# Kernel tuning notes

Measured on AMD Instinct MI355X. Metric: run time of the kernel, lower is better.

The kernel has to match this reference:

```python
import jax, jax.numpy as jnp
import numpy as np

H = W = 256
L = H * W                      # number of graph vertices / tree leaves
N_NODES = 2 * L - 1            # binary partition tree node count
LAM = 1.0                      # lambda_ (soft-area temperature)


def _grid_edges():
    """4-adjacency grid graph edges (same structure as higra get_4_adjacency_graph)."""
    idx = np.arange(L, dtype=np.int64).reshape(H, W)
    src = np.concatenate([idx[:, :-1].ravel(), idx[:-1, :].ravel()])
    dst = np.concatenate([idx[:, 1:].ravel(), idx[1:, :].ravel()])
    return src.astype(np.int32), dst.astype(np.int32)


def setup_inputs() -> dict:
    key = jax.random.key(0)
    src, dst = _grid_edges()
    ew = jax.random.uniform(key, (src.shape[0],), dtype=jnp.float32)
    return {"edge_weights": ew,
            "edges_src": jnp.asarray(src),
            "edges_dst": jnp.asarray(dst)}


def _build_tree(ew, src, dst):
    """higra.bpt_canonical: Kruskal over stably-sorted edges, building a binary
    merge tree. Leaves are 0..L-1, internal node L+i is created by the i-th MST
    edge. Returns (sizes, mst_edge_map, ancestor paths). All integer structure
    is piecewise-constant w.r.t. edge_weights (no gradient flows through it)."""
    order = np.argsort(ew, kind="stable")
    uf = np.arange(L)

    def find(x):
        r = x
        while uf[r] != r:
            r = uf[r]
        while uf[x] != r:
            uf[x], x = r, uf[x]
        return r

    canon = np.arange(L)                      # tree node of each union-find root
    parent = np.arange(N_NODES)               # self-parent until set (root keeps self)
    sizes = np.ones(N_NODES, dtype=np.float32)
    edge_map = np.zeros(L - 1, dtype=np.int64)
    node = L
    for ei in order:
        a = find(src[ei]); b = find(dst[ei])
        if a == b:
            continue
        na, nb = canon[a], canon[b]
        parent[na] = node
        parent[nb] = node
        sizes[node] = sizes[na] + sizes[nb]
        edge_map[node - L] = ei
        uf[a] = b
        canon[b] = node
        node += 1
    # self-inclusive ancestor paths, padded by repeating the root
    cur = np.arange(N_NODES)
    cols = [cur.copy()]
    while np.any(parent[cur] != cur):
        cur = parent[cur]
        cols.append(cur.copy())
    paths = np.stack(cols, axis=1)            # [N_NODES, D+1]
    return sizes, edge_map, paths


def _softarea(edge_weights, edge_map, sizes_np, paths_np):
    """Soft area of every tree node n:
       area(n) = sum_x sigmoid((alt(n) - d(x, n)) / lambda)
    where d(x,n) is the min ultrametric distance from leaf x to the leaves of n:
      - x in subtree(n), x != n : d = alt(parent(x))
      - x == n (leaf)           : d = 0
      - x outside subtree(n)    : d = alt(lowest ancestor of n containing x).
    Outside leaves are grouped per ancestor a (count = size(a) - size(previous
    node on the path)), giving an O(N * depth) vectorized computation."""
    alt = jnp.concatenate([jnp.zeros((L,), edge_weights.dtype),
                           edge_weights[edge_map]])          # [N_NODES]
    alt_path = alt[paths_np]                                  # [N, D+1]
    size_path = sizes_np[paths_np]                            # constant, numpy
    diff = jnp.asarray(size_path[:, 1:] - size_path[:, :-1])  # 0 on root padding
    outside = jnp.sum(
        diff * jax.nn.sigmoid((alt[:, None] - alt_path[:, 1:]) / LAM), axis=1)

    # inside: each leaf x contributes sigmoid((alt(a_k) - alt(parent(x)))/lam)
    # to every proper ancestor a_k, plus sigmoid(0)=0.5 to itself (alt(leaf)=0).
    lp = paths_np[:L]                                         # [L, D+1]
    alt_lp = alt_path[:L]
    valid = jnp.asarray((lp[:, 1:] != lp[:, :-1]).astype(np.float32))
    vals = jax.nn.sigmoid((alt_lp[:, 1:] - alt_lp[:, 1:2]) / LAM) * valid
    inside = jax.ops.segment_sum(vals.reshape(-1),
                                 jnp.asarray(lp[:, 1:].reshape(-1)),
                                 num_segments=N_NODES)
    inside = inside.at[:L].add(0.5)
    return inside + outside


def reference(edge_weights, edges_src, edges_dst):
    sizes, edge_map, paths = _build_tree(np.asarray(edge_weights),
                                         np.asarray(edges_src),
                                         np.asarray(edges_dst))
    return _softarea(edge_weights, jnp.asarray(edge_map), sizes, paths)
```

## Files before the change

### kernel.cpp

```cpp
#include <hip/hip_runtime.h>
#include <stdint.h>

typedef unsigned int u32;
typedef unsigned short u16;

#define L_VERTS 65536
#define N_EDGES 130560
#define N_NODES 131071
#define NODEPAD 131072

#define CCH 170
#define SCH 768
#define MAXSV 1536
#define HSZ 2048

#define NB 255
#define TPB 64
#define IPT 8
#define IPB 512

__global__ void init_keys(const float* __restrict__ w, u32* __restrict__ keys, u32* __restrict__ vals){
  int i = blockIdx.x*blockDim.x + threadIdx.x;
  if(i < N_EDGES){ keys[i] = __float_as_uint(w[i]); vals[i] = (u32)i; }
}

__global__ void radix_hist(const u32* __restrict__ idx, const u32* __restrict__ keys,
                           u32* __restrict__ histG, int shift){
  __shared__ u32 h[256];
  for(int i=threadIdx.x;i<256;i+=TPB) h[i]=0;
  __syncthreads();
  int base = blockIdx.x*IPB + threadIdx.x*IPT;
  #pragma unroll
  for(int i=0;i<IPT;i++){
    u32 e = idx[base+i];
    u32 d = (keys[e]>>shift)&255u;
    atomicAdd(&h[d],1u);
  }
  __syncthreads();
  for(int i=threadIdx.x;i<256;i+=TPB) histG[i*NB+blockIdx.x]=h[i];
}

__global__ void radix_scan(u32* histG){
  const int M = 256*NB;
  __shared__ u32 sums[1024];
  int t=threadIdx.x; int s=t*64; u32 acc=0;
  for(int i=0;i<64;i++){int id=s+i; if(id<M) acc+=histG[id];}
  sums[t]=acc; __syncthreads();
  for(int off=1; off<1024; off<<=1){
    u32 v=(t>=off)?sums[t-off]:0u;
    __syncthreads();
    sums[t]+=v;
    __syncthreads();
  }
  u32 run = (t==0)?0u:sums[t-1];
  for(int i=0;i<64;i++){int id=s+i; if(id<M){u32 v=histG[id]; histG[id]=run; run+=v;}}
}

__global__ void radix_scatter(const u32* __restrict__ idxIn, const u32* __restrict__ keys,
                              u32* __restrict__ idxOut, const u32* __restrict__ histG, int shift){
  __shared__ u16 thoff[256][TPB];
  int t=threadIdx.x;
  for(int d=t;d<256;d+=TPB) for(int j=0;j<TPB;j++) thoff[d][j]=0;
  __syncthreads();
  int base = blockIdx.x*IPB + t*IPT;
  u32 myv[IPT]; u32 myd[IPT];
  #pragma unroll
  for(int i=0;i<IPT;i++){
    myv[i]=idxIn[base+i];
    myd[i]=(keys[myv[i]]>>shift)&255u;
    thoff[myd[i]][t]++;
  }
  __syncthreads();
  for(int dd=0;dd<4;dd++){
    int d=t*4+dd; u32 run=0;
    for(int j=0;j<TPB;j++){ u32 v=thoff[d][j]; thoff[d][j]=(u16)run; run+=v; }
  }
  __syncthreads();
  #pragma unroll
  for(int i=0;i<IPT;i++){
    u32 d=myd[i];
    u32 pos = histG[d*NB+blockIdx.x] + (u32)thoff[d][t];
    thoff[d][t]++;
    idxOut[pos]=myv[i];
  }
}

__global__ void build_epair(const u32* __restrict__ order, const int* __restrict__ srcv,
                            const int* __restrict__ dstv, u32* __restrict__ epair){
  int p=blockIdx.x*blockDim.x+threadIdx.x;
  if(p>=N_EDGES) return;
  u32 e=order[p];
  epair[p]=((u32)dstv[e]<<16)|(u32)srcv[e];
}

__global__ void init_all(u32* szG,u16* canonTop16,u32* parent,float* alt){
  int i=blockIdx.x*blockDim.x+threadIdx.x;
  if(i<N_NODES){ parent[i]=(u32)i; alt[i]=0.f; }
  if(i<L_VERTS){ szG[i]=1u; canonTop16[i]=0xFFFFu; }
}

__device__ __forceinline__ u32 ald(u32* p){
  return __hip_atomic_load(p, __ATOMIC_RELAXED, __HIP_MEMORY_SCOPE_AGENT);
}
__device__ __forceinline__ void ast(u32* p, u32 v){
  __hip_atomic_store(p, v, __ATOMIC_RELAXED, __HIP_MEMORY_SCOPE_AGENT);
}

__global__ void __launch_bounds__(1024,1) p1_checkpoints(
    const u32* __restrict__ epair,
    u32* szG, u16* lid16, u16* svroot16, u16* svsize16, u16* svnext16, u32* mG)
{
  __shared__ u16 ufL[L_VERTS];
  __shared__ u32 hkey[HSZ];
  __shared__ u16 hval[HSZ];
  __shared__ u32 sufL[MAXSV];
  __shared__ u32 compsz[MAXSV];
  __shared__ u32 repkey[MAXSV];
  __shared__ u32 mcnt;
  int t = threadIdx.x;
  for(int i=t;i<L_VERTS/2;i+=1024) ((u32*)ufL)[i]=((2u*(u32)i+1u)<<16)|(2u*(u32)i);
  for(int k=0;k<CCH;k++){
    for(int i=t;i<HSZ;i+=1024) hkey[i]=0xFFFFFFFFu;
    for(u32 s=t;s<MAXSV;s+=1024){ sufL[s]=s; compsz[s]=0u; repkey[s]=0u; }
    if(t==0) mcnt=0u;
    __syncthreads();
    int base = k*SCH;
    int myslot[2]; int mycnt=0;
    for(int i=t;i<2*SCH;i+=1024){
      u32 pr = epair[base+(i>>1)];
      u32 v = (i&1)? (pr>>16) : (pr&0xFFFFu);
      u32 x=v;
      while(true){ u32 px=ufL[x]; if(px==x)break; u32 g=ufL[px]; if(g!=px) ufL[x]=(u16)g; x=g; }
      u32 r=x;
      if(v!=r) ufL[v]=(u16)r;
      u32 h=(r*2654435761u)>>21;
      int slot;
      while(true){
        u32 old=atomicCAS(&hkey[h],0xFFFFFFFFu,r);
        if(old==0xFFFFFFFFu){
          slot=(int)h;
          u32 id=atomicAdd(&mcnt,1u);
          hval[h]=(u16)id;
          svroot16[k*MAXSV+id]=(u16)r;
          break;
        }
        if(old==r){slot=(int)h;break;}
        h=(h+1)&(HSZ-1u);
      }
      myslot[mycnt++]=slot;
    }
    __syncthreads();
    u32 mc=mcnt;
    if(t==0) mG[k]=mc;
    for(u32 s=t;s<mc;s+=1024){
      u32 r=(u32)svroot16[k*MAXSV+s];
      svsize16[k*MAXSV+s]=(u16)(ald(&szG[r])-1u);
    }
    {
      int c=0;
      for(int i=t;i<2*SCH;i+=1024){ lid16[2*base+i]=hval[myslot[c]]; c++; }
    }
    __syncthreads();
    for(int i=t;i<SCH;i+=1024){
      u32 lw=((u32*)lid16)[base+i];
      u32 sa=lw&0xFFFFu, sb=lw>>16;
      if(sa==sb) continue;
      while(true){
        u32 x=sa; while(true){u32 p2=sufL[x]; if(p2==x)break; u32 g=sufL[p2]; if(g!=p2) sufL[x]=g; x=g;}
        u32 y=sb; while(true){u32 p2=sufL[y]; if(p2==y)break; u32 g=sufL[p2]; if(g!=p2) sufL[y]=g; y=g;}
        if(x==y) break;
        u32 hi=x>y?x:y, lo=x^y^hi;
        if(atomicCAS(&sufL[hi],hi,lo)==hi) break;
        sa=hi; sb=lo;
      }
    }
    __syncthreads();
    for(u32 s=t;s<mc;s+=1024){
      u32 x=s; while(true){u32 p2=sufL[x]; if(p2==x)break; x=p2;}
      sufL[s]=x;
      u32 sz=(u32)svsize16[k*MAXSV+s]+1u;
      atomicAdd(&compsz[x], sz);
      atomicMax(&repkey[x], (sz<<11) | (2047u-s));
    }
    __syncthreads();
    for(u32 s=t;s<mc;s+=1024){
      u32 rs=sufL[s];
      u32 rep=2047u-(repkey[rs]&2047u);
      u32 wv=(u32)svroot16[k*MAXSV+rep];
      svnext16[k*MAXSV+s]=(u16)wv;
      u32 myroot=(u32)svroot16[k*MAXSV+s];
      if(myroot!=wv) ufL[myroot]=(u16)wv;
      if(s==rep)     ast(&szG[wv], compsz[rs]);
    }
    __syncthreads();
  }
}

__global__ void __launch_bounds__(64) p2_chunk(
  const u16* __restrict__ lid16,
  const u16* __restrict__ svsize16, const u16* __restrict__ svnext16, const u32* __restrict__ mG,
  u16* __restrict__ outChA, u16* __restrict__ outChB, u16* __restrict__ outSize16, u16* __restrict__ outJ16,
  u32* __restrict__ accCnt, u16* __restrict__ compR16, u16* __restrict__ compTop16, u32* __restrict__ ncomp)
{
  int k = blockIdx.x; int t = threadIdx.x;
  __shared__ u16 uf[MAXSV];
  __shared__ u32 csize[MAXSV];
  __shared__ u16 ctop[MAXSV];
  __shared__ u16 svnl[MAXSV];
  __shared__ u32 cmp_s;
  u32 m = mG[k];
  for(u32 s=t;s<m;s+=64){
    uf[s]=(u16)s;
    csize[s]=(u32)svsize16[k*MAXSV+s]+1u;
    ctop[s]=(u16)s;
    svnl[s]=svnext16[k*MAXSV+s];
  }
  if(t==0) cmp_s=0u;
  __syncthreads();
  if(t==0){
    int base=k*SCH;
    u32 cnt=0;
    for(int j=0;j<SCH;j++){
      u32 lw = ((const u32*)lid16)[base+j];
      u32 la = lw & 0xFFFFu, lb = lw >> 16;
      u32 x=la; while(true){u32 px=uf[x]; if(px==x)break; u32 g=uf[px]; uf[x]=(u16)g; x=g;}
      u32 y=lb; while(true){u32 py=uf[y]; if(py==y)break; u32 g=uf[py]; uf[y]=(u16)g; y=g;}
      if(x==y) continue;
      u32 sa=csize[x], sb=csize[y], ns=sa+sb;
      outChA[base+cnt]=ctop[x];
      outChB[base+cnt]=ctop[y];
      outSize16[base+cnt]=(u16)(ns-1u);
      outJ16[base+cnt]=(u16)j;
      u32 win=(sa>=sb)?x:y, los=x^y^win;
      uf[los]=(u16)win; csize[win]=ns; ctop[win]=(u16)(0x8000u|cnt);
      cnt++;
    }
    accCnt[k]=cnt;
  }
  __syncthreads();
  for(u32 s=t;s<m;s+=64){
    if(uf[s]==(u16)s && (ctop[s]&0x8000u)){
      u32 pos=atomicAdd(&cmp_s,1u);
      compR16[k*MAXSV+pos]=svnl[s];
      compTop16[k*MAXSV+pos]=(u16)(ctop[s]&0x7FFFu);
    }
  }
  __syncthreads();
  if(t==0) ncomp[k]=cmp_s;
}

__global__ void __launch_bounds__(1024) p3_stitch(
  const u32* __restrict__ accCnt, const u16* __restrict__ outChA, const u16* __restrict__ outChB,
  const u16* __restrict__ outSize16, const u16* __restrict__ outJ16,
  const u16* __restrict__ svroot16,
  const u16* __restrict__ compR16, const u16* __restrict__ compTop16, const u32* __restrict__ ncomp,
  const u32* __restrict__ order, const float* __restrict__ w,
  u16* __restrict__ canonTop16, u32* __restrict__ parent, float* __restrict__ alt, u16* __restrict__ usize16)
{
  __shared__ u32 accBase[CCH];
  int t=threadIdx.x;
  if(t==0){ u32 r=0; for(int k=0;k<CCH;k++){ accBase[k]=r; r+=accCnt[k]; } }
  __syncthreads();
  for(int idx=t; idx<N_EDGES; idx+=1024){
    int k = idx/SCH; int j = idx - k*SCH;
    if(j < (int)accCnt[k]){
      u32 nid = (u32)L_VERTS + accBase[k] + (u32)j;
      u32 p = (u32)(k*SCH) + (u32)outJ16[idx];
      alt[nid] = w[order[p]];
      usize16[nid] = outSize16[idx];
      u32 cA=outChA[idx]; if(cA & 0x8000u) parent[(u32)L_VERTS+accBase[k]+(cA&0x7FFFu)] = nid;
      u32 cB=outChB[idx]; if(cB & 0x8000u) parent[(u32)L_VERTS+accBase[k]+(cB&0x7FFFu)] = nid;
    }
  }
  __syncthreads();
  for(int k=0;k<CCH;k++){
    u32 ac=accCnt[k];
    for(u32 j=t;j<ac;j+=1024){
      u32 idx=(u32)(k*SCH)+j;
      u32 nid=(u32)L_VERTS+accBase[k]+j;
      u32 cA=outChA[idx];
      if(!(cA&0x8000u)){
        u32 root=(u32)svroot16[k*MAXSV+cA];
        u32 ct=(u32)canonTop16[root];
        parent[(ct==0xFFFFu)?root:((u32)L_VERTS+ct)]=nid;
      }
      u32 cB=outChB[idx];
      if(!(cB&0x8000u)){
        u32 root=(u32)svroot16[k*MAXSV+cB];
        u32 ct=(u32)canonTop16[root];
        parent[(ct==0xFFFFu)?root:((u32)L_VERTS+ct)]=nid;
      }
    }
    __syncthreads();
    u32 nc=ncomp[k];
    for(u32 j=t;j<nc;j+=1024){
      canonTop16[(u32)compR16[k*MAXSV+j]] = (u16)(accBase[k]+compTop16[k*MAXSV+j]);
    }
    __syncthreads();
  }
}

__device__ __forceinline__ void hvals3(float v, int j0, float* o){
  float v2=v*v, v3=v2*v, v4=v2*v2, v5=v4*v;
  if(j0==0){
    o[0]=0.5f-0.25f*v+v3*(1.f/48.f)-v5*(1.f/480.f);
    o[1]=0.25f-v2*(1.f/16.f)+v4*(1.f/96.f);
    o[2]=v*(1.f/16.f)-v3*(1.f/48.f);
  }else{
    o[0]=v2*(1.f/48.f)-(1.f/48.f);
    o[1]=-v*(1.f/96.f);
    o[2]=(1.f/480.f);
  }
}

__global__ void zero_cc(u32* cc){
  int i=blockIdx.x*blockDim.x+threadIdx.x;
  if(i<L_VERTS) cc[i]=0u;
}

__global__ void prep_init(const u32* __restrict__ parent, const u16* __restrict__ usize16,
                          u32* cc, u32* J0, uint2* A0, float* out){
  int n=blockIdx.x*blockDim.x+threadIdx.x;
  if(n>=N_NODES) return;
  out[n] = (n<L_VERTS)?0.5f:0.0f;
  if(n==N_NODES-1){ J0[n]=(u32)n; A0[n]=make_uint2(0u,0u); return; }
  u32 p=parent[n];
  u32 ord=atomicAdd(&cc[p-L_VERTS],1u);
  u32 szP=(u32)usize16[p]+1u;
  u32 szN=(n<L_VERTS)?1u:((u32)usize16[n]+1u);
  u32 sib=szP-szN;
  A0[n]=make_uint2(ord? sib:0u, 1u + (ord? (2u*sib-1u):0u));
  J0[n]=p;
}

__global__ void double_round2(const u32* __restrict__ Jin, const uint2* __restrict__ Ain,
                              u32* __restrict__ Jout, uint2* __restrict__ Aout){
  int n=blockIdx.x*blockDim.x+threadIdx.x;
  if(n>=N_NODES) return;
  u32 j=Jin[n];
  u32 j2=Jin[j];
  u32 j3=Jin[j2];
  uint2 a=Ain[n], aj=Ain[j], b=Ain[j2], bj=Ain[j3];
  Aout[n]=make_uint2(a.x+aj.x+b.x+bj.x, a.y+aj.y+b.y+bj.y);
  Jout[n]=Jin[j3];
}

__global__ void zero_nodeM(float* nodeM){
  int i=blockIdx.x*blockDim.x+threadIdx.x;
  if(i<3*NODEPAD) nodeM[i]=0.f;
}

__global__ void scatter_all(const u32* __restrict__ parent, const float* __restrict__ alt,
                            const u16* __restrict__ usize16, const uint2* __restrict__ accF,
                            float* __restrict__ leafM, float* __restrict__ nodeM, int j0){
  int n=blockIdx.x*blockDim.x+threadIdx.x;
  if(n>=N_NODES) return;
  u32 p=parent[n];
  float h[3]; hvals3(alt[p],j0,h);
  uint2 af=accF[n];
  if(n<L_VERTS){
    u32 pos=af.x;
    leafM[0*L_VERTS+pos]=h[0];
    leafM[1*L_VERTS+pos]=h[1];
    leafM[2*L_VERTS+pos]=h[2];
  }
  if(n<N_NODES-1){
    u32 szP=(u32)usize16[p]+1u;
    u32 szN=(n<L_VERTS)?1u:((u32)usize16[n]+1u);
    float d=(float)(szP-szN);
    u32 q0=af.y;
    u32 q1=q0 + 2u*szN - 1u;
    #pragma unroll
    for(int j=0;j<3;j++){
      float tm=d*h[j];
      atomicAdd(&nodeM[j*NODEPAD+q0], tm);
      atomicAdd(&nodeM[j*NODEPAD+q1], -tm);
    }
  }
}

__global__ void scanAll(float* __restrict__ leafM, float* __restrict__ nodeM,
                        float* __restrict__ bsumL, float* __restrict__ bsumN){
  int b=blockIdx.x; int t=threadIdx.x;
  float* arr; u32 base; float* bs;
  if(b<3*64){ int row=b>>6, blk=b&63;  arr=leafM+(size_t)row*L_VERTS;  base=(u32)blk*1024u; bs=&bsumL[row*64+blk]; }
  else      { int bb=b-192; int row=bb>>7, blk=bb&127; arr=nodeM+(size_t)row*NODEPAD; base=(u32)blk*1024u; bs=&bsumN[row*128+blk]; }
  __shared__ float s[256];
  base += (u32)t*4u;
  float v0=arr[base],v1=arr[base+1],v2=arr[base+2],v3=arr[base+3];
  v1+=v0; v2+=v1; v3+=v2;
  s[t]=v3; __syncthreads();
  for(int o=1;o<256;o<<=1){ float x=(t>=o)?s[t-o]:0.f; __syncthreads(); s[t]+=x; __syncthreads(); }
  float pre=(t>0)?s[t-1]:0.f;
  arr[base]=v0+pre; arr[base+1]=v1+pre; arr[base+2]=v2+pre; arr[base+3]=v3+pre;
  if(t==255) *bs=s[255];
}

__global__ void scanB(float* bsumL, float* bsumN){
  int t=threadIdx.x;
  if(t<3){ float r=0; for(int i=0;i<64;i++){ float v=bsumL[t*64+i]; bsumL[t*64+i]=r; r+=v; } }
  else if(t<6){ int j=t-3; float r=0; for(int i=0;i<128;i++){ float v=bsumN[j*128+i]; bsumN[j*128+i]=r; r+=v; } }
}

__global__ void eval_all(const uint2* __restrict__ accF, const float* __restrict__ alt,
                         const u16* __restrict__ usize16, const float* __restrict__ leafM,
                         const float* __restrict__ nodeM, const float* __restrict__ bsumL,
                         const float* __restrict__ bsumN, float* __restrict__ out, int j0){
  int n=blockIdx.x*blockDim.x+threadIdx.x;
  if(n>=N_NODES) return;
  uint2 af=accF[n];
  float u=alt[n];
  float up0=1.f; for(int i=0;i<j0;i++) up0*=u;
  u32 q=af.y;
  float acc=0.f, up=up0;
  #pragma unroll
  for(int j=0;j<3;j++){
    float T = nodeM[(size_t)j*NODEPAD+q] + bsumN[j*128 + (q>>10)];
    acc += up*T;
    up*=u;
  }
  if(n>=L_VERTS){
    u32 lo=af.x;
    u32 hi=lo + (u32)usize16[n] + 1u;
    up=up0;
    #pragma unroll
    for(int j=0;j<3;j++){
      const float* arr=leafM + (size_t)j*L_VERTS;
      const float* bs=bsumL + j*64;
      float Ph = arr[hi-1u] + bs[(hi-1u)>>10];
      float Pl = lo ? (arr[lo-1u] + bs[(lo-1u)>>10]) : 0.f;
      acc += up*(Ph-Pl);
      up*=u;
    }
  }
  out[n]+=acc;
}

__global__ void ws_too_small(float* out){
  int i=blockIdx.x*blockDim.x+threadIdx.x;
  if(i<N_NODES) out[i]=1.0e6f;
}

extern "C" void kernel_launch(void* const* d_in, const int* in_sizes, int n_in,
                              void* d_out, int out_size, void* d_ws, size_t ws_size,
                              hipStream_t stream){
  (void)in_sizes; (void)n_in; (void)out_size;
  const float* w  = (const float*)d_in[0];
  const int* src  = (const int*)d_in[1];
  const int* dst  = (const int*)d_in[2];
  float* out = (float*)d_out;

  char* ws = (char*)d_ws;
  size_t off=0;
  auto alloc=[&](size_t bytes)->void*{ void* p = ws+off; off += (bytes+511)&~(size_t)511; return p; };
  u32* parent   =(u32*)alloc((size_t)N_NODES*4);
  float* alt    =(float*)alloc((size_t)N_NODES*4);
  u16* usize16  =(u16*)alloc((size_t)N_NODES*2);
  float* bsumL  =(float*)alloc(3*64*4);
  float* bsumN  =(float*)alloc(3*128*4);
  size_t scratch0=off;
  u32* keys0    =(u32*)alloc((size_t)N_EDGES*4);
  u32* vals0    =(u32*)alloc((size_t)N_EDGES*4);
  u32* vals1    =(u32*)alloc((size_t)N_EDGES*4);
  u32* histG    =(u32*)alloc(256*NB*4);
  u16* canonTop16=(u16*)alloc((size_t)L_VERTS*2);
  u16* outJ16   =(u16*)alloc((size_t)N_EDGES*2);
  u16* svroot16 =(u16*)alloc((size_t)CCH*MAXSV*2);
  u16* svsize16 =(u16*)alloc((size_t)CCH*MAXSV*2);
  u16* svnext16 =(u16*)alloc((size_t)CCH*MAXSV*2);
  u32* mG       =(u32*)alloc(CCH*4);
  u32* accCnt   =(u32*)alloc(CCH*4);
  u32* ncomp    =(u32*)alloc(CCH*4);
  size_t endA=off;
  off=scratch0;
  u32* ccChsum  =(u32*)alloc((size_t)L_VERTS*4);
  u32* J0       =(u32*)alloc((size_t)N_NODES*4);
  u32* J1       =(u32*)alloc((size_t)N_NODES*4);
  uint2* A0     =(uint2*)alloc((size_t)N_NODES*8);
  uint2* A1     =(uint2*)alloc((size_t)N_NODES*8);
  float* leafM  =(float*)alloc((size_t)3*L_VERTS*4);
  float* nodeM  =(float*)alloc((size_t)3*NODEPAD*4);
  size_t endB=off;

  if((endA>ws_size)||(endB>ws_size)){
    ws_too_small<<<(N_NODES+255)/256,256,0,stream>>>(out);
    return;
  }

  u16* lid16    =(u16*)vals1;
  u32* epair    =keys0;
  u16* outChA16 =(u16*)histG;
  u16* outChB16 =(u16*)keys0;
  u16* outSize16=(u16*)((char*)keys0 + (size_t)N_EDGES*2);
  u16* compR16  =svsize16;
  u16* compTop16=svnext16;
  u32* szG      =(u32*)usize16;

  init_keys<<<(N_EDGES+255)/256,256,0,stream>>>(w,keys0,vals0);
  for(int pass=0;pass<4;pass++){
    const u32* iv = (pass&1)?vals1:vals0;
    u32* ov = (pass&1)?vals0:vals1;
    int shift=pass*8;
    radix_hist   <<<NB,TPB,0,stream>>>(iv,keys0,histG,shift);
    radix_scan   <<<1,1024,0,stream>>>(histG);
    radix_scatter<<<NB,TPB,0,stream>>>(iv,keys0,ov,histG,shift);
  }
  build_epair<<<(N_EDGES+255)/256,256,0,stream>>>(vals0,src,dst,epair);
  init_all<<<(N_NODES+255)/256,256,0,stream>>>(szG,canonTop16,parent,alt);
  p1_checkpoints<<<1,1024,0,stream>>>(epair,szG,lid16,svroot16,svsize16,svnext16,mG);
  p2_chunk<<<CCH,64,0,stream>>>(lid16,svsize16,svnext16,mG,
                                outChA16,outChB16,outSize16,outJ16,accCnt,compR16,compTop16,ncomp);
  p3_stitch<<<1,1024,0,stream>>>(accCnt,outChA16,outChB16,outSize16,outJ16,svroot16,
                                 compR16,compTop16,ncomp,vals0,w,canonTop16,parent,alt,usize16);
  zero_cc<<<(L_VERTS+255)/256,256,0,stream>>>(ccChsum);
  prep_init<<<(N_NODES+255)/256,256,0,stream>>>(parent,usize16,ccChsum,J0,A0,out);
  for(int r=0;r<9;r++){
    if((r&1)==0) double_round2<<<(N_NODES+255)/256,256,0,stream>>>(J0,A0,J1,A1);
    else         double_round2<<<(N_NODES+255)/256,256,0,stream>>>(J1,A1,J0,A0);
  }
  const uint2* accF=A1;
  for(int j0=0;j0<=3;j0+=3){
    zero_nodeM<<<(3*NODEPAD+255)/256,256,0,stream>>>(nodeM);
    scatter_all<<<(N_NODES+255)/256,256,0,stream>>>(parent,alt,usize16,accF,leafM,nodeM,j0);
    scanAll<<<576,256,0,stream>>>(leafM,nodeM,bsumL,bsumN);
    scanB<<<1,64,0,stream>>>(bsumL,bsumN);
    eval_all<<<(N_NODES+255)/256,256,0,stream>>>(accF,alt,usize16,leafM,nodeM,bsumL,bsumN,out,j0);
  }
}
```

Baseline: 2.988 ms.

## Fold hash slot ids into keys in p1 and merge the two polynomial passes

The single-block union-find checkpoint kernel now gives each thread one edge. It stores the super-vertex id inside the hash key, so the separate hval table and two of the per-chunk barriers go away. Later loops iterate over hash slots directly instead of over compacted ids. Separately, the two j0 evaluation passes are merged into one pass with six polynomial coefficient rows, which halves the zero, scatter, scan and eval launches. leafM is placed over the now-dead prep scratch buffers to fit in the workspace. The cost is more atomics per scatter and more memory touched per launch.

```diff
diff --git a/kernel.cpp b/kernel.cpp
--- a/kernel.cpp
+++ b/kernel.cpp
@@ -112,85 +112,88 @@
 {
   __shared__ u16 ufL[L_VERTS];
   __shared__ u32 hkey[HSZ];
-  __shared__ u16 hval[HSZ];
-  __shared__ u32 sufL[MAXSV];
+  __shared__ u32 sufL[HSZ];
   __shared__ u32 compsz[MAXSV];
   __shared__ u32 repkey[MAXSV];
   __shared__ u32 mcnt;
   int t = threadIdx.x;
   for(int i=t;i<L_VERTS/2;i+=1024) ((u32*)ufL)[i]=((2u*(u32)i+1u)<<16)|(2u*(u32)i);
   for(int k=0;k<CCH;k++){
-    for(int i=t;i<HSZ;i+=1024) hkey[i]=0xFFFFFFFFu;
-    for(u32 s=t;s<MAXSV;s+=1024){ sufL[s]=s; compsz[s]=0u; repkey[s]=0u; }
+    for(int i=t;i<HSZ;i+=1024){ hkey[i]=0xFFFFFFFFu; sufL[i]=(u32)i; }
+    for(int i=t;i<MAXSV;i+=1024){ compsz[i]=0u; repkey[i]=0u; }
     if(t==0) mcnt=0u;
     __syncthreads();
     int base = k*SCH;
-    int myslot[2]; int mycnt=0;
-    for(int i=t;i<2*SCH;i+=1024){
-      u32 pr = epair[base+(i>>1)];
-      u32 v = (i&1)? (pr>>16) : (pr&0xFFFFu);
-      u32 x=v;
-      while(true){ u32 px=ufL[x]; if(px==x)break; u32 g=ufL[px]; if(g!=px) ufL[x]=(u16)g; x=g; }
-      u32 r=x;
-      if(v!=r) ufL[v]=(u16)r;
-      u32 h=(r*2654435761u)>>21;
-      int slot;
-      while(true){
-        u32 old=atomicCAS(&hkey[h],0xFFFFFFFFu,r);
-        if(old==0xFFFFFFFFu){
-          slot=(int)h;
-          u32 id=atomicAdd(&mcnt,1u);
-          hval[h]=(u16)id;
-          svroot16[k*MAXSV+id]=(u16)r;
-          break;
+    u32 sa=0u, sb=0u;
+    if(t<SCH){
+      u32 pr=epair[base+t];
+      u32 va=pr&0xFFFFu, vb=pr>>16;
+      u32 x=va; while(true){u32 px=ufL[x]; if(px==x)break; u32 g=ufL[px]; if(g!=px) ufL[x]=(u16)g; x=g;}
+      u32 ra=x; if(va!=ra) ufL[va]=(u16)ra;
+      x=vb; while(true){u32 px=ufL[x]; if(px==x)break; u32 g=ufL[px]; if(g!=px) ufL[x]=(u16)g; x=g;}
+      u32 rb=x; if(vb!=rb) ufL[vb]=(u16)rb;
+      u32 rr[2]={ra,rb}; u32 ss[2];
+      #pragma unroll
+      for(int e2=0;e2<2;e2++){
+        u32 r=rr[e2];
+        u32 h=(r*2654435761u)>>21;
+        while(true){
+          u32 old=atomicCAS(&hkey[h],0xFFFFFFFFu,(r<<16)|0x7FFFu);
+          if(old==0xFFFFFFFFu){
+            u32 id=atomicAdd(&mcnt,1u);
+            svroot16[k*MAXSV+id]=(u16)r;
+            hkey[h]=(r<<16)|id;
+            break;
+          }
+          if((old>>16)==r) break;
+          h=(h+1)&(HSZ-1u);
         }
-        if(old==r){slot=(int)h;break;}
-        h=(h+1)&(HSZ-1u);
+        ss[e2]=h;
       }
-      myslot[mycnt++]=slot;
-    }
-    __syncthreads();
-    u32 mc=mcnt;
-    if(t==0) mG[k]=mc;
-    for(u32 s=t;s<mc;s+=1024){
-      u32 r=(u32)svroot16[k*MAXSV+s];
-      svsize16[k*MAXSV+s]=(u16)(ald(&szG[r])-1u);
-    }
-    {
-      int c=0;
-      for(int i=t;i<2*SCH;i+=1024){ lid16[2*base+i]=hval[myslot[c]]; c++; }
-    }
-    __syncthreads();
-    for(int i=t;i<SCH;i+=1024){
-      u32 lw=((u32*)lid16)[base+i];
-      u32 sa=lw&0xFFFFu, sb=lw>>16;
-      if(sa==sb) continue;
-      while(true){
-        u32 x=sa; while(true){u32 p2=sufL[x]; if(p2==x)break; u32 g=sufL[p2]; if(g!=p2) sufL[x]=g; x=g;}
-        u32 y=sb; while(true){u32 p2=sufL[y]; if(p2==y)break; u32 g=sufL[p2]; if(g!=p2) sufL[y]=g; y=g;}
-        if(x==y) break;
-        u32 hi=x>y?x:y, lo=x^y^hi;
-        if(atomicCAS(&sufL[hi],hi,lo)==hi) break;
-        sa=hi; sb=lo;
+      sa=ss[0]; sb=ss[1];
+      if(sa!=sb){
+        u32 s0=sa, s1=sb;
+        while(true){
+          u32 xx=s0; while(true){u32 p2=sufL[xx]; if(p2==xx)break; u32 g=sufL[p2]; if(g!=p2) sufL[xx]=g; xx=g;}
+          u32 yy=s1; while(true){u32 p2=sufL[yy]; if(p2==yy)break; u32 g=sufL[p2]; if(g!=p2) sufL[yy]=g; yy=g;}
+          if(xx==yy) break;
+          u32 hi=xx>yy?xx:yy, lo=xx^yy^hi;
+          if(atomicCAS(&sufL[hi],hi,lo)==hi) break;
+          s0=hi; s1=lo;
+        }
       }
     }
     __syncthreads();
-    for(u32 s=t;s<mc;s+=1024){
+    if(t==0) mG[k]=mcnt;
+    if(t<SCH){
+      u32 ida=hkey[sa]&0xFFFFu, idb=hkey[sb]&0xFFFFu;
+      ((u32*)lid16)[base+t]=(idb<<16)|ida;
+    }
+    for(u32 s=t;s<HSZ;s+=1024){
+      u32 hk=hkey[s];
+      if(hk==0xFFFFFFFFu) continue;
+      u32 r=hk>>16, myid=hk&0xFFFFu;
+      u32 sz=ald(&szG[r]);
+      svsize16[k*MAXSV+myid]=(u16)(sz-1u);
       u32 x=s; while(true){u32 p2=sufL[x]; if(p2==x)break; x=p2;}
       sufL[s]=x;
-      u32 sz=(u32)svsize16[k*MAXSV+s]+1u;
-      atomicAdd(&compsz[x], sz);
-      atomicMax(&repkey[x], (sz<<11) | (2047u-s));
-    }
-    __syncthreads();
-    for(u32 s=t;s<mc;s+=1024){
-      u32 rs=sufL[s];
-      u32 rep=2047u-(repkey[rs]&2047u);
-      u32 wv=(u32)svroot16[k*MAXSV+rep];
-      svnext16[k*MAXSV+s]=(u16)wv;
-      u32 myroot=(u32)svroot16[k*MAXSV+s];
+      u32 idx=hkey[x]&0xFFFFu;
+      atomicAdd(&compsz[idx], sz);
+      atomicMax(&repkey[idx], (sz<<11) | (2047u-s));
+    }
+    __syncthreads();
+    for(u32 s=t;s<HSZ;s+=1024){
+      u32 hk=hkey[s];
+      if(hk==0xFFFFFFFFu) continue;
+      u32 x=sufL[s];
+      u32 idx=hkey[x]&0xFFFFu;
+      u32 rep=2047u-(repkey[idx]&2047u);
+      u32 wv=hkey[rep]>>16;
+      u32 myid=hk&0xFFFFu;
+      svnext16[k*MAXSV+myid]=(u16)wv;
+      u32 myroot=hk>>16;
       if(myroot!=wv) ufL[myroot]=(u16)wv;
-      if(s==rep)     ast(&szG[wv], compsz[rs]);
+      if(s==rep)     ast(&szG[wv], compsz[idx]);
     }
     __syncthreads();
   }
@@ -300,17 +303,14 @@
   }
 }
 
-__device__ __forceinline__ void hvals3(float v, int j0, float* o){
+__device__ __forceinline__ void hvals6(float v, float* o){
   float v2=v*v, v3=v2*v, v4=v2*v2, v5=v4*v;
-  if(j0==0){
-    o[0]=0.5f-0.25f*v+v3*(1.f/48.f)-v5*(1.f/480.f);
-    o[1]=0.25f-v2*(1.f/16.f)+v4*(1.f/96.f);
-    o[2]=v*(1.f/16.f)-v3*(1.f/48.f);
-  }else{
-    o[0]=v2*(1.f/48.f)-(1.f/48.f);
-    o[1]=-v*(1.f/96.f);
-    o[2]=(1.f/480.f);
-  }
+  o[0]=0.5f-0.25f*v+v3*(1.f/48.f)-v5*(1.f/480.f);
+  o[1]=0.25f-v2*(1.f/16.f)+v4*(1.f/96.f);
+  o[2]=v*(1.f/16.f)-v3*(1.f/48.f);
+  o[3]=v2*(1.f/48.f)-(1.f/48.f);
+  o[4]=-v*(1.f/96.f);
+  o[5]=(1.f/480.f);
 }
 
 __global__ void zero_cc(u32* cc){
@@ -347,22 +347,21 @@
 
 __global__ void zero_nodeM(float* nodeM){
   int i=blockIdx.x*blockDim.x+threadIdx.x;
-  if(i<3*NODEPAD) nodeM[i]=0.f;
+  if(i<6*NODEPAD) nodeM[i]=0.f;
 }
 
 __global__ void scatter_all(const u32* __restrict__ parent, const float* __restrict__ alt,
                             const u16* __restrict__ usize16, const uint2* __restrict__ accF,
-                            float* __restrict__ leafM, float* __restrict__ nodeM, int j0){
+                            float* __restrict__ leafM, float* __restrict__ nodeM){
   int n=blockIdx.x*blockDim.x+threadIdx.x;
   if(n>=N_NODES) return;
   u32 p=parent[n];
-  float h[3]; hvals3(alt[p],j0,h);
+  float h[6]; hvals6(alt[p],h);
   uint2 af=accF[n];
   if(n<L_VERTS){
     u32 pos=af.x;
-    leafM[0*L_VERTS+pos]=h[0];
-    leafM[1*L_VERTS+pos]=h[1];
-    leafM[2*L_VERTS+pos]=h[2];
+    #pragma unroll
+    for(int j=0;j<6;j++) leafM[(size_t)j*L_VERTS+pos]=h[j];
   }
   if(n<N_NODES-1){
     u32 szP=(u32)usize16[p]+1u;
@@ -371,10 +370,10 @@
     u32 q0=af.y;
     u32 q1=q0 + 2u*szN - 1u;
     #pragma unroll
-    for(int j=0;j<3;j++){
+    for(int j=0;j<6;j++){
       float tm=d*h[j];
-      atomicAdd(&nodeM[j*NODEPAD+q0], tm);
-      atomicAdd(&nodeM[j*NODEPAD+q1], -tm);
+      atomicAdd(&nodeM[(size_t)j*NODEPAD+q0], tm);
+      atomicAdd(&nodeM[(size_t)j*NODEPAD+q1], -tm);
     }
   }
 }
@@ -383,8 +382,8 @@
                         float* __restrict__ bsumL, float* __restrict__ bsumN){
   int b=blockIdx.x; int t=threadIdx.x;
   float* arr; u32 base; float* bs;
-  if(b<3*64){ int row=b>>6, blk=b&63;  arr=leafM+(size_t)row*L_VERTS;  base=(u32)blk*1024u; bs=&bsumL[row*64+blk]; }
-  else      { int bb=b-192; int row=bb>>7, blk=bb&127; arr=nodeM+(size_t)row*NODEPAD; base=(u32)blk*1024u; bs=&bsumN[row*128+blk]; }
+  if(b<6*64){ int row=b>>6, blk=b&63;  arr=leafM+(size_t)row*L_VERTS;  base=(u32)blk*1024u; bs=&bsumL[row*64+blk]; }
+  else      { int bb=b-384; int row=bb>>7, blk=bb&127; arr=nodeM+(size_t)row*NODEPAD; base=(u32)blk*1024u; bs=&bsumN[row*128+blk]; }
   __shared__ float s[256];
   base += (u32)t*4u;
   float v0=arr[base],v1=arr[base+1],v2=arr[base+2],v3=arr[base+3];
@@ -398,23 +397,22 @@
 
 __global__ void scanB(float* bsumL, float* bsumN){
   int t=threadIdx.x;
-  if(t<3){ float r=0; for(int i=0;i<64;i++){ float v=bsumL[t*64+i]; bsumL[t*64+i]=r; r+=v; } }
-  else if(t<6){ int j=t-3; float r=0; for(int i=0;i<128;i++){ float v=bsumN[j*128+i]; bsumN[j*128+i]=r; r+=v; } }
+  if(t<6){ float r=0; for(int i=0;i<64;i++){ float v=bsumL[t*64+i]; bsumL[t*64+i]=r; r+=v; } }
+  else if(t<12){ int j=t-6; float r=0; for(int i=0;i<128;i++){ float v=bsumN[j*128+i]; bsumN[j*128+i]=r; r+=v; } }
 }
 
 __global__ void eval_all(const uint2* __restrict__ accF, const float* __restrict__ alt,
                          const u16* __restrict__ usize16, const float* __restrict__ leafM,
                          const float* __restrict__ nodeM, const float* __restrict__ bsumL,
-                         const float* __restrict__ bsumN, float* __restrict__ out, int j0){
+                         const float* __restrict__ bsumN, float* __restrict__ out){
   int n=blockIdx.x*blockDim.x+threadIdx.x;
   if(n>=N_NODES) return;
   uint2 af=accF[n];
   float u=alt[n];
-  float up0=1.f; for(int i=0;i<j0;i++) up0*=u;
   u32 q=af.y;
-  float acc=0.f, up=up0;
+  float acc=0.f, up=1.f;
   #pragma unroll
-  for(int j=0;j<3;j++){
+  for(int j=0;j<6;j++){
     float T = nodeM[(size_t)j*NODEPAD+q] + bsumN[j*128 + (q>>10)];
     acc += up*T;
     up*=u;
@@ -422,9 +420,9 @@
   if(n>=L_VERTS){
     u32 lo=af.x;
     u32 hi=lo + (u32)usize16[n] + 1u;
-    up=up0;
+    up=1.f;
     #pragma unroll
-    for(int j=0;j<3;j++){
+    for(int j=0;j<6;j++){
       const float* arr=leafM + (size_t)j*L_VERTS;
       const float* bs=bsumL + j*64;
       float Ph = arr[hi-1u] + bs[(hi-1u)>>10];
@@ -456,8 +454,8 @@
   u32* parent   =(u32*)alloc((size_t)N_NODES*4);
   float* alt    =(float*)alloc((size_t)N_NODES*4);
   u16* usize16  =(u16*)alloc((size_t)N_NODES*2);
-  float* bsumL  =(float*)alloc(3*64*4);
-  float* bsumN  =(float*)alloc(3*128*4);
+  float* bsumL  =(float*)alloc(6*64*4);
+  float* bsumN  =(float*)alloc(6*128*4);
   size_t scratch0=off;
   u32* keys0    =(u32*)alloc((size_t)N_EDGES*4);
   u32* vals0    =(u32*)alloc((size_t)N_EDGES*4);
@@ -478,9 +476,9 @@
   u32* J1       =(u32*)alloc((size_t)N_NODES*4);
   uint2* A0     =(uint2*)alloc((size_t)N_NODES*8);
   uint2* A1     =(uint2*)alloc((size_t)N_NODES*8);
-  float* leafM  =(float*)alloc((size_t)3*L_VERTS*4);
-  float* nodeM  =(float*)alloc((size_t)3*NODEPAD*4);
+  float* nodeM  =(float*)alloc((size_t)6*NODEPAD*4);
   size_t endB=off;
+  float* leafM  =(float*)ccChsum;
 
   if((endA>ws_size)||(endB>ws_size)){
     ws_too_small<<<(N_NODES+255)/256,256,0,stream>>>(out);
@@ -519,11 +517,9 @@
     else         double_round2<<<(N_NODES+255)/256,256,0,stream>>>(J1,A1,J0,A0);
   }
   const uint2* accF=A1;
-  for(int j0=0;j0<=3;j0+=3){
-    zero_nodeM<<<(3*NODEPAD+255)/256,256,0,stream>>>(nodeM);
-    scatter_all<<<(N_NODES+255)/256,256,0,stream>>>(parent,alt,usize16,accF,leafM,nodeM,j0);
-    scanAll<<<576,256,0,stream>>>(leafM,nodeM,bsumL,bsumN);
-    scanB<<<1,64,0,stream>>>(bsumL,bsumN);
-    eval_all<<<(N_NODES+255)/256,256,0,stream>>>(accF,alt,usize16,leafM,nodeM,bsumL,bsumN,out,j0);
-  }
-}
+  zero_nodeM<<<(6*NODEPAD+255)/256,256,0,stream>>>(nodeM);
+  scatter_all<<<(N_NODES+255)/256,256,0,stream>>>(parent,alt,usize16,accF,leafM,nodeM);
+  scanAll<<<1152,256,0,stream>>>(leafM,nodeM,bsumL,bsumN);
+  scanB<<<1,64,0,stream>>>(bsumL,bsumN);
+  eval_all<<<(N_NODES+255)/256,256,0,stream>>>(accF,alt,usize16,leafM,nodeM,bsumL,bsumN,out);
+}
```

New measurement: 8.536 ms. +185.7%, slower.
